# Performance work log

Measured on AMD Instinct MI355X. Metric: run time of the kernel, lower is better.

## Reference

```python
import jax, jax.numpy as jnp
import numpy as np

GRID = 128  # grid_size from init_kwargs


def _splat(coords2, alpha, feats):
    """Alpha-weighted splat of per-point features onto a GRIDxGRID plane.
    coords2: [N,2] normalized coords in [-1,1]; alpha: [N]; feats: [N,C].
    Returns [C, GRID, GRID].
    """
    g = ((coords2 * 0.5 + 0.5) * (GRID - 1)).astype(jnp.int32)  # trunc like torch .long()
    g = jnp.clip(g, 0, GRID - 1)
    idx = g[:, 0] * GRID + g[:, 1]  # [N]
    num = jax.ops.segment_sum(feats * alpha[:, None], idx, num_segments=GRID * GRID)  # [G2,C]
    den = jnp.maximum(jax.ops.segment_sum(alpha, idx, num_segments=GRID * GRID), 1e-6)  # [G2]
    C = feats.shape[-1]
    return (num / den[:, None]).T.reshape(C, GRID, GRID)


def setup_inputs() -> dict:
    key = jax.random.key(0)
    k1, _ = jax.random.split(key)
    B, N, C = 4, 131072, 196
    GS_feats = jax.random.normal(k1, (B, N, C), dtype=jnp.float32)
    scene_bounds = jnp.arange(6, dtype=jnp.float32)  # (0,1,2,3,4,5) -> unit extents
    return {"GS_feats": GS_feats, "scene_bounds": scene_bounds}


def reference(GS_feats, scene_bounds):
    lo = scene_bounds[jnp.array([0, 2, 4])]  # [3]
    hi = scene_bounds[jnp.array([1, 3, 5])]  # [3]
    coords_n = 2.0 * (GS_feats[..., :3] - lo) / (hi - lo) - 1.0  # [B,N,3]
    feats = jnp.concatenate([coords_n, GS_feats[..., 3:]], axis=-1)  # [B,N,C]
    alpha = jax.nn.sigmoid(feats[..., 3])  # [B,N]
    # plane coord pairs: xy, xz, yz -> [B,3,N,2]
    plane_coords = jnp.stack(
        [coords_n[..., jnp.array([0, 1])],
         coords_n[..., jnp.array([0, 2])],
         coords_n[..., jnp.array([1, 2])]], axis=1)
    splat_planes = jax.vmap(_splat, in_axes=(0, None, None))  # over the 3 planes
    splat_batch = jax.vmap(splat_planes, in_axes=(0, 0, 0))   # over batch
    return splat_batch(plane_coords, alpha, feats)  # [B,3,C,GRID,GRID]
```

## Files before the change

### kernel.cpp

```cpp
#include <hip/hip_runtime.h>
#include <math.h>

#define GRID_SZ 128
#define NC 196
#define NC4 49
#define G2 (GRID_SZ*GRID_SZ)
#define BPB 64
#define SLOTS 128
#define SLOTF 200
#define AW 16


__device__ __forceinline__ void lds_flush(float* __restrict__ tbl, int tag,
                                          float v0, float v1, float v2, float v3,
                                          float d, int lane, bool l4) {
    float* slot = tbl + tag * SLOTF;
    atomicAdd(slot + lane, v0);
    atomicAdd(slot + 64 + lane, v1);
    atomicAdd(slot + 128 + lane, v2);
    if (l4) atomicAdd(slot + 192 + lane, v3);
    if (lane == 4) atomicAdd(slot + 196, d);
}

__global__ __launch_bounds__(1024, 1) void lds_accum_kernel(
    const float* __restrict__ gs, const float* __restrict__ sb,
    float* __restrict__ nw, float* __restrict__ dn,
    float* __restrict__ tblout, int N) {
    __shared__ float tbl[SLOTS * SLOTF];

    const int tid = threadIdx.x;
    const int lane = tid & 63;
    const int widx = tid >> 6;

    for (int i = tid; i < SLOTS * SLOTF; i += 1024) tbl[i] = 0.f;
    __syncthreads();

    const int b = blockIdx.x / BPB;
    const int blk = blockIdx.x % BPB;
    const int strip = N / BPB;
    const int cnt = strip / AW;
    const long long p0 = (long long)b * N + (long long)blk * strip
                       + (long long)widx * cnt;

    const float lo0 = sb[0], hi0 = sb[1];
    const float lo1 = sb[2], hi1 = sb[3];
    const float lo2 = sb[4], hi2 = sb[5];
    const float s0 = 2.0f / (hi0 - lo0);
    const float s1 = 2.0f / (hi1 - lo1);
    const float s2 = 2.0f / (hi2 - lo2);

    const float* rows = gs + (size_t)p0 * NC;
    const bool l4 = (lane < 4);

    #define LOADP(J, V0, V1, V2, V3)                                   \
        {                                                              \
            const float* r_ = rows + (size_t)(J) * NC;                 \
            V0 = r_[lane];                                             \
            V1 = r_[64 + lane];                                        \
            V2 = r_[128 + lane];                                       \
            V3 = l4 ? r_[192 + lane] : 0.f;                            \
        }

    float vA0, vA1, vA2, vA3, vB0, vB1, vB2, vB3;
    float vC0, vC1, vC2, vC3, vD0, vD1, vD2, vD3;
    float vE0, vE1, vE2, vE3, vF0, vF1, vF2, vF3;
    float vG0, vG1, vG2, vG3, vH0, vH1, vH2, vH3;
    {
        const int i1 = (1 < cnt) ? 1 : cnt - 1;
        const int i2 = (2 < cnt) ? 2 : cnt - 1;
        const int i3 = (3 < cnt) ? 3 : cnt - 1;
        const int i4 = (4 < cnt) ? 4 : cnt - 1;
        const int i5 = (5 < cnt) ? 5 : cnt - 1;
        const int i6 = (6 < cnt) ? 6 : cnt - 1;
        const int i7 = (7 < cnt) ? 7 : cnt - 1;
        LOADP(0, vA0, vA1, vA2, vA3);
        LOADP(i1, vB0, vB1, vB2, vB3);
        LOADP(i2, vC0, vC1, vC2, vC3);
        LOADP(i3, vD0, vD1, vD2, vD3);
        LOADP(i4, vE0, vE1, vE2, vE3);
        LOADP(i5, vF0, vF1, vF2, vF3);
        LOADP(i6, vG0, vG1, vG2, vG3);
        LOADP(i7, vH0, vH1, vH2, vH3);
    }

    float z0 = 0.f, z1 = 0.f, z2 = 0.f, z3 = 0.f, zd = 0.f;
    float y0 = 0.f, y1 = 0.f, y2 = 0.f, y3 = 0.f, yd = 0.f;
    int ctag = -1;
    float cc0 = 0.f, cc1 = 0.f, cc2 = 0.f, cc3 = 0.f, ccd = 0.f;

    #define CONSUME(V0, V1, V2, V3)                                          \
        {                                                                    \
            const float hx = __shfl(V0, 0);                                  \
            const float hy = __shfl(V0, 1);                                  \
            const float hz = __shfl(V0, 2);                                  \
            const float hw = __shfl(V0, 3);                                  \
            const float cnx = (hx - lo0) * s0 - 1.0f;                        \
            const float cny = (hy - lo1) * s1 - 1.0f;                        \
            const float cnz = (hz - lo2) * s2 - 1.0f;                        \
            int gx = (int)((cnx * 0.5f + 0.5f) * 127.0f);                    \
            int gy = (int)((cny * 0.5f + 0.5f) * 127.0f);                    \
            int gz = (int)((cnz * 0.5f + 0.5f) * 127.0f);                    \
            gx = min(127, max(0, gx));                                       \
            gy = min(127, max(0, gy));                                       \
            gz = min(127, max(0, gz));                                       \
            const float alpha = 1.0f / (1.0f + __expf(-hw));                 \
            float v0 = V0;                                                   \
            if (lane == 0) v0 = cnx;                                         \
            else if (lane == 1) v0 = cny;                                    \
            else if (lane == 2) v0 = cnz;                                    \
            const float av0 = v0 * alpha;                                    \
            const float av1 = (V1) * alpha;                                  \
            const float av2 = (V2) * alpha;                                  \
            const float av3 = (V3) * alpha;                                  \
            if ((gy | gz) == 0) {                                            \
                if (gx == 0) {                                               \
                    z0 += av0; z1 += av1; z2 += av2; z3 += av3; zd += alpha; \
                } else if (gx == 127) {                                      \
                    y0 += av0; y1 += av1; y2 += av2; y3 += av3; yd += alpha; \
                } else if (gx == ctag) {                                     \
                    cc0 += av0; cc1 += av1; cc2 += av2; cc3 += av3;          \
                    ccd += alpha;                                            \
                } else {                                                     \
                    if (ctag > 0)                                            \
                        lds_flush(tbl, ctag, cc0, cc1, cc2, cc3, ccd,        \
                                  lane, l4);                                 \
                    ctag = gx;                                               \
                    cc0 = av0; cc1 = av1; cc2 = av2; cc3 = av3;              \
                    ccd = alpha;                                             \
                }                                                            \
            } else {                                                         \
                const int cells[3] = { gx * GRID_SZ + gy, gx * GRID_SZ + gz, \
                                       gy * GRID_SZ + gz };                  \
                _Pragma("unroll")                                            \
                for (int p = 0; p < 3; ++p) {                                \
                    const int bin = (b * 3 + p) * G2 + cells[p];             \
                    float* dst = nw + (size_t)bin * NC;                      \
                    unsafeAtomicAdd(dst + lane, av0);                        \
                    unsafeAtomicAdd(dst + 64 + lane, av1);                   \
                    unsafeAtomicAdd(dst + 128 + lane, av2);                  \
                    if (l4) unsafeAtomicAdd(dst + 192 + lane, av3);          \
                    if (lane == 4) unsafeAtomicAdd(dn + bin, alpha);         \
                }                                                            \
            }                                                                \
        }

    for (int j = 0; j < cnt; j += 4) {
        float vI0, vI1, vI2, vI3, vJ0, vJ1, vJ2, vJ3;
        float vK0, vK1, vK2, vK3, vL0, vL1, vL2, vL3;
        const int j8  = (j + 8  < cnt) ? j + 8  : cnt - 1;
        const int j9  = (j + 9  < cnt) ? j + 9  : cnt - 1;
        const int j10 = (j + 10 < cnt) ? j + 10 : cnt - 1;
        const int j11 = (j + 11 < cnt) ? j + 11 : cnt - 1;
        LOADP(j8, vI0, vI1, vI2, vI3);
        LOADP(j9, vJ0, vJ1, vJ2, vJ3);
        LOADP(j10, vK0, vK1, vK2, vK3);
        LOADP(j11, vL0, vL1, vL2, vL3);

        CONSUME(vA0, vA1, vA2, vA3);
        CONSUME(vB0, vB1, vB2, vB3);
        CONSUME(vC0, vC1, vC2, vC3);
        CONSUME(vD0, vD1, vD2, vD3);

        vA0 = vE0; vA1 = vE1; vA2 = vE2; vA3 = vE3;
        vB0 = vF0; vB1 = vF1; vB2 = vF2; vB3 = vF3;
        vC0 = vG0; vC1 = vG1; vC2 = vG2; vC3 = vG3;
        vD0 = vH0; vD1 = vH1; vD2 = vH2; vD3 = vH3;
        vE0 = vI0; vE1 = vI1; vE2 = vI2; vE3 = vI3;
        vF0 = vJ0; vF1 = vJ1; vF2 = vJ2; vF3 = vJ3;
        vG0 = vK0; vG1 = vK1; vG2 = vK2; vG3 = vK3;
        vH0 = vL0; vH1 = vL1; vH2 = vL2; vH3 = vL3;
    }
    #undef CONSUME
    #undef LOADP

    if (ctag > 0) lds_flush(tbl, ctag, cc0, cc1, cc2, cc3, ccd, lane, l4);
    lds_flush(tbl, 127, y0, y1, y2, y3, yd, lane, l4);
    lds_flush(tbl, 0, z0, z1, z2, z3, zd, lane, l4);

    __syncthreads();
    for (int i = tid; i < SLOTS * SLOTF; i += 1024) {
        const int s = i / SLOTF;
        const int f = i - s * SLOTF;
        tblout[(((size_t)b * SLOTS + s) * BPB + blk) * SLOTF + f] = tbl[i];
    }
}


__global__ __launch_bounds__(256) void table_reduce_kernel(
    const float* __restrict__ tblout,
    float* __restrict__ nw, float* __restrict__ dn, int B) {
    const int lane = threadIdx.x & 63;
    const int w = blockIdx.x * 4 + (threadIdx.x >> 6);
    if (w >= B * SLOTS) return;
    const int b = w >> 7;
    const int gx = w & 127;
    const bool l4 = (lane < 4);

    const float* base = tblout + ((size_t)(b * SLOTS + gx) * BPB) * SLOTF;
    float a0 = 0.f, a1 = 0.f, a2 = 0.f, a3 = 0.f, den = 0.f;
    for (int r = 0; r < BPB; ++r) {
        const float* rec = base + (size_t)r * SLOTF;
        a0 += rec[lane];
        a1 += rec[64 + lane];
        a2 += rec[128 + lane];
        if (l4) a3 += rec[192 + lane];
        if (lane == 4) den += rec[196];
    }

    const int cells[3] = { gx * GRID_SZ, gx * GRID_SZ, 0 };
    #pragma unroll
    for (int p = 0; p < 3; ++p) {
        const int bin = (b * 3 + p) * G2 + cells[p];
        float* dst = nw + (size_t)bin * NC;
        unsafeAtomicAdd(dst + lane, a0);
        unsafeAtomicAdd(dst + 64 + lane, a1);
        unsafeAtomicAdd(dst + 128 + lane, a2);
        if (l4) unsafeAtomicAdd(dst + 192 + lane, a3);
        if (lane == 4) unsafeAtomicAdd(dn + bin, den);
    }
}


#define TCELLS 64
__global__ __launch_bounds__(256) void xpose_kernel(const float* __restrict__ nw,
                                                    const float* __restrict__ dn,
                                                    float* __restrict__ out) {
    __shared__ float tile[TCELLS][197];
    __shared__ float dinv[TCELLS];
    const int t = threadIdx.x;
    const int pg = blockIdx.x >> 8;
    const int c0 = (blockIdx.x & 255) * TCELLS;

    const float* src = nw + ((size_t)pg * G2 + c0) * NC;
    for (int i = t; i < TCELLS * NC4; i += 256) {
        const int cell = i / NC4;
        const int cp = i - cell * NC4;
        float4 v = ((const float4*)(src + (size_t)cell * NC))[cp];
        float* dst = &tile[cell][cp * 4];
        dst[0] = v.x; dst[1] = v.y; dst[2] = v.z; dst[3] = v.w;
    }
    if (t < TCELLS) dinv[t] = 1.0f / fmaxf(dn[pg * G2 + c0 + t], 1e-6f);
    __syncthreads();

    float* obase = out + (size_t)pg * NC * G2 + c0;
    for (int i = t; i < TCELLS * NC; i += 256) {
        const int c = i >> 6;
        const int cell = i & 63;
        obase[(size_t)c * G2 + cell] = tile[cell][c] * dinv[cell];
    }
}


__global__ void zero_kernel(float4* __restrict__ p, long long n4) {
    long long i = (long long)blockIdx.x * blockDim.x + threadIdx.x;
    long long stride = (long long)gridDim.x * blockDim.x;
    const float4 z = make_float4(0.f, 0.f, 0.f, 0.f);
    for (; i < n4; i += stride) p[i] = z;
}


struct Slot { int tag; float den; float4 acc; };

__device__ __forceinline__ void slot_flush(const Slot& s, float* __restrict__ out,
                                           float* __restrict__ den,
                                           size_t outPlaneBase, int denPlaneBase, int lane) {
    if (s.tag < 0) return;
    if (lane < NC4) {
        size_t base = outPlaneBase + (size_t)(4 * lane) * G2 + (size_t)s.tag;
        unsafeAtomicAdd(out + base,                s.acc.x);
        unsafeAtomicAdd(out + base + (size_t)G2,   s.acc.y);
        unsafeAtomicAdd(out + base + (size_t)2*G2, s.acc.z);
        unsafeAtomicAdd(out + base + (size_t)3*G2, s.acc.w);
    }
    if (lane == 0) unsafeAtomicAdd(den + denPlaneBase + s.tag, s.den);
}

__device__ __forceinline__ void plane_acc(Slot& a, Slot& b, int cell, float alpha,
                                          const float4& av,
                                          float* __restrict__ out, float* __restrict__ den,
                                          size_t outPlaneBase, int denPlaneBase, int lane) {
    if (cell == a.tag) {
        a.acc.x += av.x; a.acc.y += av.y; a.acc.z += av.z; a.acc.w += av.w; a.den += alpha;
    } else if (cell == b.tag) {
        b.acc.x += av.x; b.acc.y += av.y; b.acc.z += av.z; b.acc.w += av.w; b.den += alpha;
    } else {
        if (b.den > a.den) { Slot t = a; a = b; b = t; }
        slot_flush(b, out, den, outPlaneBase, denPlaneBase, lane);
        b.tag = cell; b.den = alpha; b.acc = av;
    }
}

__global__ __launch_bounds__(256) void splat_kernel(
    const float* __restrict__ gs, const float* __restrict__ sb,
    float* __restrict__ out, float* __restrict__ den, int B, int N, int ppw) {
    const int lane = threadIdx.x & 63;
    const long long wave = (long long)blockIdx.x * (blockDim.x >> 6) + (threadIdx.x >> 6);
    const long long totalPts = (long long)B * N;
    long long start = wave * ppw;
    if (start >= totalPts) return;
    long long end = start + ppw;
    if (end > totalPts) end = totalPts;
    const int bb = (int)(start / N);

    const float lo0 = sb[0], hi0 = sb[1];
    const float lo1 = sb[2], hi1 = sb[3];
    const float lo2 = sb[4], hi2 = sb[5];
    const float s0 = 2.0f / (hi0 - lo0);
    const float s1 = 2.0f / (hi1 - lo1);
    const float s2 = 2.0f / (hi2 - lo2);

    const size_t ob0 = ((size_t)(bb * 3 + 0) * NC) * G2;
    const size_t ob1 = ((size_t)(bb * 3 + 1) * NC) * G2;
    const size_t ob2 = ((size_t)(bb * 3 + 2) * NC) * G2;
    const int db0 = (bb * 3 + 0) * G2;
    const int db1 = (bb * 3 + 1) * G2;
    const int db2 = (bb * 3 + 2) * G2;

    const float4 f40 = make_float4(0.f, 0.f, 0.f, 0.f);
    Slot a0{-1,0.f,f40}, t0{-1,0.f,f40}, a1{-1,0.f,f40}, t1{-1,0.f,f40},
         a2{-1,0.f,f40}, t2{-1,0.f,f40};

    const float4* rows = (const float4*)gs;
    const float4* r0 = rows + (size_t)start * NC4;
    float4 v = (lane < NC4) ? r0[lane] : f40;
    float4 h = r0[0];

    for (long long i = start; i < end; ++i) {
        float4 vn = f40, hn = f40;
        if (i + 1 < end) {
            const float4* rn = rows + (size_t)(i + 1) * NC4;
            vn = (lane < NC4) ? rn[lane] : f40;
            hn = rn[0];
        }
        const float cnx = (h.x - lo0) * s0 - 1.0f;
        const float cny = (h.y - lo1) * s1 - 1.0f;
        const float cnz = (h.z - lo2) * s2 - 1.0f;
        int gx = (int)((cnx * 0.5f + 0.5f) * 127.0f);
        int gy = (int)((cny * 0.5f + 0.5f) * 127.0f);
        int gz = (int)((cnz * 0.5f + 0.5f) * 127.0f);
        gx = min(127, max(0, gx)); gy = min(127, max(0, gy)); gz = min(127, max(0, gz));
        const int cxy = __builtin_amdgcn_readfirstlane(gx * GRID_SZ + gy);
        const int cxz = __builtin_amdgcn_readfirstlane(gx * GRID_SZ + gz);
        const int cyz = __builtin_amdgcn_readfirstlane(gy * GRID_SZ + gz);
        const float alpha = 1.0f / (1.0f + __expf(-h.w));
        float4 vv = v;
        if (lane == 0) { vv.x = cnx; vv.y = cny; vv.z = cnz; }
        const float4 av = make_float4(vv.x*alpha, vv.y*alpha, vv.z*alpha, vv.w*alpha);
        plane_acc(a0, t0, cxy, alpha, av, out, den, ob0, db0, lane);
        plane_acc(a1, t1, cxz, alpha, av, out, den, ob1, db1, lane);
        plane_acc(a2, t2, cyz, alpha, av, out, den, ob2, db2, lane);
        v = vn; h = hn;
    }
    slot_flush(a0, out, den, ob0, db0, lane);
    slot_flush(t0, out, den, ob0, db0, lane);
    slot_flush(a1, out, den, ob1, db1, lane);
    slot_flush(t1, out, den, ob1, db1, lane);
    slot_flush(a2, out, den, ob2, db2, lane);
    slot_flush(t2, out, den, ob2, db2, lane);
}

__global__ void normalize_kernel(float* __restrict__ out, const float* __restrict__ den,
                                 int total4) {
    int idx = blockIdx.x * blockDim.x + threadIdx.x;
    const int stride = gridDim.x * blockDim.x;
    for (; idx < total4; idx += stride) {
        float4 v = ((float4*)out)[idx];
        const int e = idx * 4;
        const int cell = e & (G2 - 1);
        const int bp = e / (NC * G2);
        const float4 d = *(const float4*)(den + bp * G2 + cell);
        v.x /= fmaxf(d.x, 1e-6f);
        v.y /= fmaxf(d.y, 1e-6f);
        v.z /= fmaxf(d.z, 1e-6f);
        v.w /= fmaxf(d.w, 1e-6f);
        ((float4*)out)[idx] = v;
    }
}


extern "C" void kernel_launch(void* const* d_in, const int* in_sizes, int n_in,
                              void* d_out, int out_size, void* d_ws, size_t ws_size,
                              hipStream_t stream) {
    const float* gs = (const float*)d_in[0];
    const float* sb = (const float*)d_in[1];
    float* out = (float*)d_out;

    const int B = out_size / (3 * NC * G2);
    const int N = (int)((long long)in_sizes[0] / ((long long)B * NC));
    const int NB = B * 3 * G2;

    const size_t nwF = (size_t)NB * NC;
    const size_t dnF = (size_t)NB;
    const size_t tblF = (size_t)B * SLOTS * BPB * SLOTF;
    size_t off = 0;
    const size_t o_nw = off;    off += nwF * 4;
    const size_t o_dn = off;    off += dnF * 4;
    const size_t o_tbl = off;   off += tblF * 4;
    const size_t need = off;

    if (ws_size >= need && (N % (BPB * AW)) == 0 && B >= 1) {
        char* ws = (char*)d_ws;
        float* nw = (float*)(ws + o_nw);
        float* dn = (float*)(ws + o_dn);
        float* tblout = (float*)(ws + o_tbl);

        zero_kernel<<<4096, 256, 0, stream>>>((float4*)nw,
                                              (long long)(nwF + dnF) / 4);

        const int aBlocks = B * BPB;
        lds_accum_kernel<<<aBlocks, 1024, 0, stream>>>(gs, sb, nw, dn, tblout, N);

        const int rWaves = B * SLOTS;
        const int rBlocks = (rWaves + 3) / 4;
        table_reduce_kernel<<<rBlocks, 256, 0, stream>>>(tblout, nw, dn, B);

        const int xblocks = B * 3 * (G2 / TCELLS);
        xpose_kernel<<<xblocks, 256, 0, stream>>>(nw, dn, out);
    } else {
        float* den = (float*)d_ws;
        const long long out4 = (long long)out_size / 4;
        const long long den4 = (long long)dnF / 4;
        const int ppw = 64;
        const long long waves = ((long long)B * N) / ppw;
        const int blocks = (int)((waves + 3) / 4);
        zero_kernel<<<2048, 256, 0, stream>>>((float4*)out, out4);
        zero_kernel<<<256, 256, 0, stream>>>((float4*)den, den4);
        splat_kernel<<<blocks, 256, 0, stream>>>(gs, sb, out, den, B, N, ppw);
        normalize_kernel<<<4096, 256, 0, stream>>>(out, den, (int)out4);
    }
}
```

Before: 354.7 us.

## Replace LDS partial table with global atomics to raise occupancy

Removes the 100KB shared-memory table from the accumulation kernel and flushes the per-block partial sums straight into the global partial-table workspace with unsafe float atomics. That workspace is now zeroed by the existing zero kernel, and the block count per batch doubles. The prefetch depth drops from eight rows to four to cut register pressure, and launch bounds now request more resident blocks. The aim is higher occupancy and no LDS init or copy-out phase, at the cost of global atomic traffic, a larger table to zero and reduce, and less load latency hiding.

Measured after the change: 444.7 us. +25.4%, slower.

```diff
diff --git a/kernel.cpp b/kernel.cpp
--- a/kernel.cpp
+++ b/kernel.cpp
@@ -5,35 +5,30 @@
 #define NC 196
 #define NC4 49
 #define G2 (GRID_SZ*GRID_SZ)
-#define BPB 64
+#define BPB 128
 #define SLOTS 128
 #define SLOTF 200
 #define AW 16
 
 
-__device__ __forceinline__ void lds_flush(float* __restrict__ tbl, int tag,
+__device__ __forceinline__ void tbl_flush(float* __restrict__ tblB, int tag,
                                           float v0, float v1, float v2, float v3,
                                           float d, int lane, bool l4) {
-    float* slot = tbl + tag * SLOTF;
-    atomicAdd(slot + lane, v0);
-    atomicAdd(slot + 64 + lane, v1);
-    atomicAdd(slot + 128 + lane, v2);
-    if (l4) atomicAdd(slot + 192 + lane, v3);
-    if (lane == 4) atomicAdd(slot + 196, d);
-}
-
-__global__ __launch_bounds__(1024, 1) void lds_accum_kernel(
+    float* slot = tblB + (size_t)tag * ((size_t)BPB * SLOTF);
+    unsafeAtomicAdd(slot + lane, v0);
+    unsafeAtomicAdd(slot + 64 + lane, v1);
+    unsafeAtomicAdd(slot + 128 + lane, v2);
+    if (l4) unsafeAtomicAdd(slot + 192 + lane, v3);
+    if (lane == 4) unsafeAtomicAdd(slot + 196, d);
+}
+
+__global__ __launch_bounds__(1024, 8) void gbl_accum_kernel(
     const float* __restrict__ gs, const float* __restrict__ sb,
     float* __restrict__ nw, float* __restrict__ dn,
     float* __restrict__ tblout, int N) {
-    __shared__ float tbl[SLOTS * SLOTF];
-
     const int tid = threadIdx.x;
     const int lane = tid & 63;
     const int widx = tid >> 6;
-
-    for (int i = tid; i < SLOTS * SLOTF; i += 1024) tbl[i] = 0.f;
-    __syncthreads();
 
     const int b = blockIdx.x / BPB;
     const int blk = blockIdx.x % BPB;
@@ -41,6 +36,8 @@
     const int cnt = strip / AW;
     const long long p0 = (long long)b * N + (long long)blk * strip
                        + (long long)widx * cnt;
+
+    float* tblB = tblout + ((size_t)b * SLOTS * BPB + blk) * SLOTF;
 
     const float lo0 = sb[0], hi0 = sb[1];
     const float lo1 = sb[2], hi1 = sb[3];
@@ -63,24 +60,14 @@
 
     float vA0, vA1, vA2, vA3, vB0, vB1, vB2, vB3;
     float vC0, vC1, vC2, vC3, vD0, vD1, vD2, vD3;
-    float vE0, vE1, vE2, vE3, vF0, vF1, vF2, vF3;
-    float vG0, vG1, vG2, vG3, vH0, vH1, vH2, vH3;
     {
         const int i1 = (1 < cnt) ? 1 : cnt - 1;
         const int i2 = (2 < cnt) ? 2 : cnt - 1;
         const int i3 = (3 < cnt) ? 3 : cnt - 1;
-        const int i4 = (4 < cnt) ? 4 : cnt - 1;
-        const int i5 = (5 < cnt) ? 5 : cnt - 1;
-        const int i6 = (6 < cnt) ? 6 : cnt - 1;
-        const int i7 = (7 < cnt) ? 7 : cnt - 1;
         LOADP(0, vA0, vA1, vA2, vA3);
         LOADP(i1, vB0, vB1, vB2, vB3);
         LOADP(i2, vC0, vC1, vC2, vC3);
         LOADP(i3, vD0, vD1, vD2, vD3);
-        LOADP(i4, vE0, vE1, vE2, vE3);
-        LOADP(i5, vF0, vF1, vF2, vF3);
-        LOADP(i6, vG0, vG1, vG2, vG3);
-        LOADP(i7, vH0, vH1, vH2, vH3);
     }
 
     float z0 = 0.f, z1 = 0.f, z2 = 0.f, z3 = 0.f, zd = 0.f;
@@ -122,7 +109,7 @@
                     ccd += alpha;                                            \
                 } else {                                                     \
                     if (ctag > 0)                                            \
-                        lds_flush(tbl, ctag, cc0, cc1, cc2, cc3, ccd,        \
+                        tbl_flush(tblB, ctag, cc0, cc1, cc2, cc3, ccd,       \
                                   lane, l4);                                 \
                     ctag = gx;                                               \
                     cc0 = av0; cc1 = av1; cc2 = av2; cc3 = av3;              \
@@ -145,16 +132,16 @@
         }
 
     for (int j = 0; j < cnt; j += 4) {
-        float vI0, vI1, vI2, vI3, vJ0, vJ1, vJ2, vJ3;
-        float vK0, vK1, vK2, vK3, vL0, vL1, vL2, vL3;
-        const int j8  = (j + 8  < cnt) ? j + 8  : cnt - 1;
-        const int j9  = (j + 9  < cnt) ? j + 9  : cnt - 1;
-        const int j10 = (j + 10 < cnt) ? j + 10 : cnt - 1;
-        const int j11 = (j + 11 < cnt) ? j + 11 : cnt - 1;
-        LOADP(j8, vI0, vI1, vI2, vI3);
-        LOADP(j9, vJ0, vJ1, vJ2, vJ3);
-        LOADP(j10, vK0, vK1, vK2, vK3);
-        LOADP(j11, vL0, vL1, vL2, vL3);
+        float vE0, vE1, vE2, vE3, vF0, vF1, vF2, vF3;
+        float vG0, vG1, vG2, vG3, vH0, vH1, vH2, vH3;
+        const int j4 = (j + 4 < cnt) ? j + 4 : cnt - 1;
+        const int j5 = (j + 5 < cnt) ? j + 5 : cnt - 1;
+        const int j6 = (j + 6 < cnt) ? j + 6 : cnt - 1;
+        const int j7 = (j + 7 < cnt) ? j + 7 : cnt - 1;
+        LOADP(j4, vE0, vE1, vE2, vE3);
+        LOADP(j5, vF0, vF1, vF2, vF3);
+        LOADP(j6, vG0, vG1, vG2, vG3);
+        LOADP(j7, vH0, vH1, vH2, vH3);
 
         CONSUME(vA0, vA1, vA2, vA3);
         CONSUME(vB0, vB1, vB2, vB3);
@@ -165,24 +152,13 @@
         vB0 = vF0; vB1 = vF1; vB2 = vF2; vB3 = vF3;
         vC0 = vG0; vC1 = vG1; vC2 = vG2; vC3 = vG3;
         vD0 = vH0; vD1 = vH1; vD2 = vH2; vD3 = vH3;
-        vE0 = vI0; vE1 = vI1; vE2 = vI2; vE3 = vI3;
-        vF0 = vJ0; vF1 = vJ1; vF2 = vJ2; vF3 = vJ3;
-        vG0 = vK0; vG1 = vK1; vG2 = vK2; vG3 = vK3;
-        vH0 = vL0; vH1 = vL1; vH2 = vL2; vH3 = vL3;
     }
     #undef CONSUME
     #undef LOADP
 
-    if (ctag > 0) lds_flush(tbl, ctag, cc0, cc1, cc2, cc3, ccd, lane, l4);
-    lds_flush(tbl, 127, y0, y1, y2, y3, yd, lane, l4);
-    lds_flush(tbl, 0, z0, z1, z2, z3, zd, lane, l4);
-
-    __syncthreads();
-    for (int i = tid; i < SLOTS * SLOTF; i += 1024) {
-        const int s = i / SLOTF;
-        const int f = i - s * SLOTF;
-        tblout[(((size_t)b * SLOTS + s) * BPB + blk) * SLOTF + f] = tbl[i];
-    }
+    if (ctag > 0) tbl_flush(tblB, ctag, cc0, cc1, cc2, cc3, ccd, lane, l4);
+    tbl_flush(tblB, 127, y0, y1, y2, y3, yd, lane, l4);
+    tbl_flush(tblB, 0, z0, z1, z2, z3, zd, lane, l4);
 }
 
 
@@ -405,10 +381,10 @@
         float* tblout = (float*)(ws + o_tbl);
 
         zero_kernel<<<4096, 256, 0, stream>>>((float4*)nw,
-                                              (long long)(nwF + dnF) / 4);
+                                              (long long)(nwF + dnF + tblF) / 4);
 
         const int aBlocks = B * BPB;
-        lds_accum_kernel<<<aBlocks, 1024, 0, stream>>>(gs, sb, nw, dn, tblout, N);
+        gbl_accum_kernel<<<aBlocks, 1024, 0, stream>>>(gs, sb, nw, dn, tblout, N);
 
         const int rWaves = B * SLOTS;
         const int rBlocks = (rWaves + 3) / 4;
```
